# Kernel optimization log

Measured on AMD Instinct MI355X. Metric: run time of the kernel, lower is better.

Reference implementation:

```python
import jax, jax.numpy as jnp
import numpy as np

GRID = 64
AABB_MIN = np.array([-1.25, -1.55, -1.25], dtype=np.float32)
AABB_MAX = np.array([1.25, 0.95, 1.25], dtype=np.float32)
DENSITY_THRESH = 0.5


def setup_inputs() -> dict:
    key = jax.random.key(0)
    ks = jax.random.split(key, 12)
    N, S, H = 8192, 128, 64
    rays_o = jax.random.normal(ks[0], (N, 3), jnp.float32) * 0.1
    d = jax.random.normal(ks[1], (N, 3), jnp.float32)
    rays_d = d / jnp.sqrt(jnp.clip(jnp.sum(d * d, -1, keepdims=True), 1e-20))
    near = 0.05 + jax.random.uniform(ks[2], (N,), jnp.float32) * 0.5
    far = near + 2.0 + jax.random.uniform(ks[3], (N,), jnp.float32) * 0.5
    jitter = jax.random.uniform(ks[4], (N, S), jnp.float32)
    density_field = jax.random.uniform(ks[5], (GRID, GRID, GRID), jnp.float32)
    W1 = jax.random.normal(ks[6], (3, H), jnp.float32) * 0.5
    b1 = jnp.zeros((H,), jnp.float32)
    W2 = jax.random.normal(ks[7], (H, H), jnp.float32) * (1.0 / np.sqrt(H))
    b2 = jnp.zeros((H,), jnp.float32)
    Wsig = jax.random.normal(ks[8], (H, 1), jnp.float32) * (1.0 / np.sqrt(H))
    bsig = jnp.zeros((1,), jnp.float32)
    Wrgb = jax.random.normal(ks[9], (H, 3), jnp.float32) * (1.0 / np.sqrt(H))
    brgb = jnp.zeros((3,), jnp.float32)
    return {"rays_o": rays_o, "rays_d": rays_d, "near": near, "far": far,
            "jitter": jitter, "density_field": density_field,
            "W1": W1, "b1": b1, "W2": W2, "b2": b2,
            "Wsig": Wsig, "bsig": bsig, "Wrgb": Wrgb, "brgb": brgb}


def _render_train(rays_o, rays_d, near, far, jitter, density_field,
                  W1, b1, W2, b2, Wsig, bsig, Wrgb, brgb):
    N, S = jitter.shape
    step = (far - near) / S                                  # [N]
    offset = jnp.asarray(AABB_MIN)
    scale = jnp.asarray(AABB_MAX) - jnp.asarray(AABB_MIN)
    # uniform march (raymarch_train): z_i = near + i*step, zeroed where grid empty
    z = near[:, None] + jnp.arange(S, dtype=jnp.float32)[None, :] * step[:, None]  # [N,S]
    pts0 = rays_o[:, None, :] + z[..., None] * rays_d[:, None, :]                  # [N,S,3]
    u = (pts0 - offset) / scale
    idx = jnp.floor(u * GRID).astype(jnp.int32)
    inb = jnp.all((idx >= 0) & (idx < GRID), axis=-1)
    idxc = jnp.clip(idx, 0, GRID - 1)
    occ = density_field[idxc[..., 0], idxc[..., 1], idxc[..., 2]] > DENSITY_THRESH
    z_vals = jnp.where(occ & inb, z, 0.0)                    # [N,S]
    mask = z_vals > 0
    # stratified jitter (torch: z_vals + rand * step_size)
    z_vals = z_vals + jitter * step[:, None]
    pts = rays_o[:, None, :] + z_vals[..., None] * rays_d[:, None, :]  # [N,S,3]
    # radiance-field MLP (stand-in for `model(pts, None)`)
    h = jax.nn.relu(jnp.einsum('nsc,ch->nsh', pts, W1) + b1)
    h = jax.nn.relu(jnp.einsum('nsh,hk->nsk', h, W2) + b2)
    sigma = (jnp.einsum('nsh,ho->nso', h, Wsig) + bsig)[..., 0]        # [N,S]
    rgb = jax.nn.sigmoid(jnp.einsum('nsh,ho->nso', h, Wrgb) + brgb)    # [N,S,3]
    # torch fills masked-out samples with sigma=-1000, rgb=0
    sigma = jnp.where(mask, sigma, -1000.0)
    rgb = jnp.where(mask[..., None], rgb, 0.0)
    # composite
    dists = jnp.broadcast_to(step[:, None], sigma.shape)
    tau = jax.nn.relu(sigma) * dists
    alpha = 1.0 - jnp.exp(-tau)
    trans = jnp.concatenate([jnp.ones_like(alpha[..., :1]),
                             jnp.cumprod(1.0 - alpha + 1e-10, axis=-1)], axis=-1)
    w = alpha * trans[..., :-1]                              # [N,S]
    no_hit = trans[..., -1]
    color = jnp.sum(w[..., None] * rgb, axis=-2) + no_hit[..., None]   # bg_color=None -> white
    depth = jnp.sum(w * z_vals, axis=-1)
    return color, depth


def reference(rays_o, rays_d, near, far, jitter, density_field,
              W1, b1, W2, b2, Wsig, bsig, Wrgb, brgb):
    color, depth = _render_train(rays_o, rays_d, near, far, jitter, density_field,
                                 W1, b1, W2, b2, Wsig, bsig, Wrgb, brgb)
    return color
```

## Files before the change

kernel.cpp:

```cpp
#include <hip/hip_runtime.h>
#include <math.h>

#define S 128
#define H 64
#define RPB 4
#define SPB (RPB * S)
#define T 256

typedef __attribute__((ext_vector_type(8))) short bf16x8;
typedef __attribute__((ext_vector_type(4))) float f32x4;
#define MFMA16(a, b, c) __builtin_amdgcn_mfma_f32_16x16x32_bf16((a), (b), (c), 0, 0, 0)

__device__ __forceinline__ short f2bf(float x) {
    unsigned u = __float_as_uint(x);
    unsigned r = (u + 0x7fffu + ((u >> 16) & 1u)) >> 16;
    return (short)r;
}

__device__ __forceinline__ bool sample_mask(
    float ox, float oy, float oz, float dx, float dy, float dz,
    float nr, float step, int s, const float* __restrict__ density)
{
    const float z  = __fadd_rn(nr, __fmul_rn((float)s, step));
    const float px = __fadd_rn(ox, __fmul_rn(z, dx));
    const float py = __fadd_rn(oy, __fmul_rn(z, dy));
    const float pz = __fadd_rn(oz, __fmul_rn(z, dz));
    const float gx = floorf(__fmul_rn(__fdiv_rn(__fsub_rn(px, -1.25f), 2.5f), 64.0f));
    const float gy = floorf(__fmul_rn(__fdiv_rn(__fsub_rn(py, -1.55f), 2.5f), 64.0f));
    const float gz = floorf(__fmul_rn(__fdiv_rn(__fsub_rn(pz, -1.25f), 2.5f), 64.0f));
    const int ix = (int)gx, iy = (int)gy, iz = (int)gz;
    const bool inb = (ix >= 0) && (ix < 64) && (iy >= 0) && (iy < 64) &&
                     (iz >= 0) && (iz < 64);
    const int cx = min(max(ix, 0), 63);
    const int cy = min(max(iy, 0), 63);
    const int cz = min(max(iz, 0), 63);
    const float dval = density[(cx << 12) | (cy << 6) | cz];
    return inb && (dval > 0.5f);
}

__global__ __launch_bounds__(256)
void fused_mfma_kernel(const float* __restrict__ rays_o, const float* __restrict__ rays_d,
                       const float* __restrict__ nearv, const float* __restrict__ farv,
                       const float* __restrict__ jitter, const float* __restrict__ density,
                       const float* __restrict__ W1, const float* __restrict__ b1,
                       const float* __restrict__ W2, const float* __restrict__ b2,
                       const float* __restrict__ Wsig, const float* __restrict__ bsig,
                       const float* __restrict__ Wrgb, const float* __restrict__ brgb,
                       float* __restrict__ out, int N)
{
    __shared__ __align__(16) short sW2[H * 68];
    __shared__ __align__(16) short h1h[4][16 * 72];
    __shared__ __align__(16) short h2b[4][16 * 72];
    __shared__ unsigned short s_list[SPB];
    __shared__ float s_alpha[SPB];
    __shared__ float s_r[SPB], s_g[SPB], s_b[SPB];
    __shared__ int s_wcnt[4];
    __shared__ int s_wbase[4];

    const int tid  = threadIdx.x;
    const int lane = tid & 63;
    const int wv   = tid >> 6;
    const int blk  = blockIdx.x;
    const int mrow = lane & 15;
    const int quad = lane >> 4;

    for (int e = tid; e < H * H; e += T) {
        const int k = e >> 6, n = e & 63;
        sW2[k * 68 + n] = f2bf(W2[e]);
    }

    const int gr    = blk * RPB + wv;
    const int lbase = tid * 2;
    unsigned int mybits = 0u;
    if (gr < N) {
        const float ox = rays_o[gr * 3 + 0], oy = rays_o[gr * 3 + 1], oz = rays_o[gr * 3 + 2];
        const float dx = rays_d[gr * 3 + 0], dy = rays_d[gr * 3 + 1], dz = rays_d[gr * 3 + 2];
        const float nr = nearv[gr];
        const float step = __fdiv_rn(__fsub_rn(farv[gr], nr), 128.0f);
        const int s0 = lane * 2;
        #pragma unroll
        for (int j = 0; j < 2; ++j) {
            const bool m = sample_mask(ox, oy, oz, dx, dy, dz, nr, step, s0 + j, density);
            if (m) {
                mybits |= (1u << j);
            } else {
                s_alpha[lbase + j] = 0.0f;
                s_r[lbase + j] = 0.0f;
                s_g[lbase + j] = 0.0f;
                s_b[lbase + j] = 0.0f;
            }
        }
    } else {
        #pragma unroll
        for (int j = 0; j < 2; ++j) {
            s_alpha[lbase + j] = 0.0f;
            s_r[lbase + j] = 0.0f;
            s_g[lbase + j] = 0.0f;
            s_b[lbase + j] = 0.0f;
        }
    }
    const int mycnt = __popc(mybits);
    int inc = mycnt;
    #pragma unroll
    for (int off = 1; off < 64; off <<= 1) {
        const int u = __shfl_up(inc, off, 64);
        if (lane >= off) inc += u;
    }
    if (lane == 63) s_wcnt[wv] = inc;
    __syncthreads();
    if (tid == 0) {
        int t0 = 0;
        #pragma unroll
        for (int i = 0; i < 4; ++i) { s_wbase[i] = t0; t0 += s_wcnt[i]; }
    }
    __syncthreads();
    int pos = s_wbase[wv] + (inc - mycnt);
    if (mybits & 1u) s_list[pos++] = (unsigned short)lbase;
    if (mybits & 2u) s_list[pos]   = (unsigned short)(lbase + 1);
    __syncthreads();
    const int K = s_wbase[3] + s_wcnt[3];

    bf16x8 w2f[4][2];
    #pragma unroll
    for (int nt = 0; nt < 4; ++nt) {
        #pragma unroll
        for (int ks = 0; ks < 2; ++ks) {
            bf16x8 f;
            #pragma unroll
            for (int j = 0; j < 8; ++j)
                f[j] = sW2[(32 * ks + 8 * quad + j) * 68 + mrow + 16 * nt];
            w2f[nt][ks] = f;
        }
    }
    bf16x8 w1f[4];
    #pragma unroll
    for (int nt = 0; nt < 4; ++nt) {
        bf16x8 f = {0, 0, 0, 0, 0, 0, 0, 0};
        if (quad == 0) {
            const int n = mrow + 16 * nt;
            f[0] = f2bf(W1[n]);
            f[1] = f2bf(W1[64 + n]);
            f[2] = f2bf(W1[128 + n]);
        }
        w1f[nt] = f;
    }
    bf16x8 a3f[2];
    #pragma unroll
    for (int ks = 0; ks < 2; ++ks) {
        bf16x8 f = {0, 0, 0, 0, 0, 0, 0, 0};
        if (mrow < 4) {
            #pragma unroll
            for (int j = 0; j < 8; ++j) {
                const int k = 32 * ks + 8 * quad + j;
                const float v = (mrow == 0) ? Wsig[k] : Wrgb[k * 3 + (mrow - 1)];
                f[j] = f2bf(v);
            }
        }
        a3f[ks] = f;
    }
    float b1v[4], b2v[4];
    #pragma unroll
    for (int nt = 0; nt < 4; ++nt) {
        b1v[nt] = b1[mrow + 16 * nt];
        b2v[nt] = b2[mrow + 16 * nt];
    }
    const float bsg = bsig[0];
    const float br0 = brgb[0], br1 = brgb[1], br2 = brgb[2];

    const f32x4 z4 = {0.f, 0.f, 0.f, 0.f};
    const int ntask = (K + 15) >> 4;
    short* const hb = &h1h[wv][0];
    short* const gb = &h2b[wv][0];

    for (int t = wv; t < ntask; t += 4) {
        const int slot = (t << 4) + mrow;
        const bool valid = slot < K;
        const int id = s_list[valid ? slot : 0];
        const int r = blk * RPB + (id >> 7);
        const int s = id & (S - 1);
        const float nr = nearv[r];
        const float step = __fdiv_rn(__fsub_rn(farv[r], nr), 128.0f);
        const float zs = __fadd_rn(nr, __fmul_rn((float)s, step));
        const float zj = zs + jitter[blk * SPB + id] * step;
        const float qx = rays_o[r * 3 + 0] + zj * rays_d[r * 3 + 0];
        const float qy = rays_o[r * 3 + 1] + zj * rays_d[r * 3 + 1];
        const float qz = rays_o[r * 3 + 2] + zj * rays_d[r * 3 + 2];

        bf16x8 ah = {0, 0, 0, 0, 0, 0, 0, 0};
        if (quad == 0) { ah[0] = f2bf(qx); ah[1] = f2bf(qy); ah[2] = f2bf(qz); }
        #pragma unroll
        for (int nt = 0; nt < 4; ++nt) {
            const f32x4 c1 = MFMA16(ah, w1f[nt], z4);
            #pragma unroll
            for (int rg = 0; rg < 4; ++rg) {
                const float v = fmaxf(c1[rg] + b1v[nt], 0.0f);
                hb[(4 * quad + rg) * 72 + mrow + 16 * nt] = f2bf(v);
            }
        }

        bf16x8 a2_0 = *(const bf16x8*)&hb[mrow * 72 + 8 * quad];
        bf16x8 a2_1 = *(const bf16x8*)&hb[mrow * 72 + 32 + 8 * quad];
        #pragma unroll
        for (int nt = 0; nt < 4; ++nt) {
            const f32x4 c2 = MFMA16(a2_1, w2f[nt][1], MFMA16(a2_0, w2f[nt][0], z4));
            #pragma unroll
            for (int rg = 0; rg < 4; ++rg) {
                const float v = fmaxf(c2[rg] + b2v[nt], 0.0f);
                gb[(4 * quad + rg) * 72 + mrow + 16 * nt] = f2bf(v);
            }
        }

        bf16x8 b3_0 = *(const bf16x8*)&gb[mrow * 72 + 8 * quad];
        bf16x8 b3_1 = *(const bf16x8*)&gb[mrow * 72 + 32 + 8 * quad];
        const f32x4 c3 = MFMA16(a3f[1], b3_1, MFMA16(a3f[0], b3_0, z4));

        if (quad == 0 && valid) {
            const float sg = c3[0] + bsg;
            const float tau = fmaxf(sg, 0.0f) * step;
            s_alpha[id] = 1.0f - expf(-tau);
            s_r[id] = 1.0f / (1.0f + expf(-(c3[1] + br0)));
            s_g[id] = 1.0f / (1.0f + expf(-(c3[2] + br1)));
            s_b[id] = 1.0f / (1.0f + expf(-(c3[3] + br2)));
        }
    }
    __syncthreads();

    if (gr < N) {
        const int b0 = wv * S + 2 * lane;
        const float2 a01 = *reinterpret_cast<const float2*>(&s_alpha[b0]);
        const float a0 = a01.x, a1 = a01.y;
        const float t0 = (1.0f - a0) + 1e-10f;
        const float t1 = (1.0f - a1) + 1e-10f;
        float v = t0 * t1;
        #pragma unroll
        for (int off = 1; off < 64; off <<= 1) {
            const float u = __shfl_up(v, off, 64);
            if (lane >= off) v *= u;
        }
        float excl = __shfl_up(v, 1, 64);
        if (lane == 0) excl = 1.0f;
        const float no_hit = __shfl(v, 63, 64);
        const float w0 = a0 * excl;
        const float w1 = a1 * (excl * t0);
        const float2 r01 = *reinterpret_cast<const float2*>(&s_r[b0]);
        const float2 g01 = *reinterpret_cast<const float2*>(&s_g[b0]);
        const float2 b01 = *reinterpret_cast<const float2*>(&s_b[b0]);
        float cr = w0 * r01.x + w1 * r01.y;
        float cg = w0 * g01.x + w1 * g01.y;
        float cb = w0 * b01.x + w1 * b01.y;
        #pragma unroll
        for (int off = 32; off >= 1; off >>= 1) {
            cr += __shfl_xor(cr, off, 64);
            cg += __shfl_xor(cg, off, 64);
            cb += __shfl_xor(cb, off, 64);
        }
        if (lane == 0) {
            out[gr * 3 + 0] = cr + no_hit;
            out[gr * 3 + 1] = cg + no_hit;
            out[gr * 3 + 2] = cb + no_hit;
        }
    }
}

extern "C" void kernel_launch(void* const* d_in, const int* in_sizes, int n_in,
                              void* d_out, int out_size, void* d_ws, size_t ws_size,
                              hipStream_t stream) {
    const float* rays_o  = (const float*)d_in[0];
    const float* rays_d  = (const float*)d_in[1];
    const float* nearv   = (const float*)d_in[2];
    const float* farv    = (const float*)d_in[3];
    const float* jitter  = (const float*)d_in[4];
    const float* density = (const float*)d_in[5];
    const float* W1      = (const float*)d_in[6];
    const float* b1      = (const float*)d_in[7];
    const float* W2      = (const float*)d_in[8];
    const float* b2      = (const float*)d_in[9];
    const float* Wsig    = (const float*)d_in[10];
    const float* bsig    = (const float*)d_in[11];
    const float* Wrgb    = (const float*)d_in[12];
    const float* brgb    = (const float*)d_in[13];
    float* out = (float*)d_out;

    const int N = in_sizes[2];

    fused_mfma_kernel<<<dim3((N + RPB - 1) / RPB), dim3(T), 0, stream>>>(
        rays_o, rays_d, nearv, farv, jitter, density,
        W1, b1, W2, b2, Wsig, bsig, Wrgb, brgb, out, N);
}
```

Measured before the change: 109.5 us.

## Process eight rays per block and transpose W2 in LDS for vector loads

Doubles the rays handled per block so each thread builds masks for four samples, and each wave composites several rays. The per-block cost of converting W2 to bf16 and loading weight fragments is paid once for twice as much work. W2 is now stored transposed in shared memory, so each MFMA B-fragment comes from one 16-byte read instead of eight scalar reads. The two hidden-layer staging buffers are merged into one to save LDS. The trade-off is half as many blocks, fewer waves available to hide latency, and more shared memory per block for the larger sample arrays.

```diff
diff --git a/kernel.cpp b/kernel.cpp
--- a/kernel.cpp
+++ b/kernel.cpp
@@ -3,7 +3,7 @@
 
 #define S 128
 #define H 64
-#define RPB 4
+#define RPB 8
 #define SPB (RPB * S)
 #define T 256
 
@@ -48,9 +48,8 @@
                        const float* __restrict__ Wrgb, const float* __restrict__ brgb,
                        float* __restrict__ out, int N)
 {
-    __shared__ __align__(16) short sW2[H * 68];
-    __shared__ __align__(16) short h1h[4][16 * 72];
-    __shared__ __align__(16) short h2b[4][16 * 72];
+    __shared__ __align__(16) short sW2t[H * 72];
+    __shared__ __align__(16) short hX[4][16 * 72];
     __shared__ unsigned short s_list[SPB];
     __shared__ float s_alpha[SPB];
     __shared__ float s_r[SPB], s_g[SPB], s_b[SPB];
@@ -66,20 +65,20 @@
 
     for (int e = tid; e < H * H; e += T) {
         const int k = e >> 6, n = e & 63;
-        sW2[k * 68 + n] = f2bf(W2[e]);
-    }
-
-    const int gr    = blk * RPB + wv;
-    const int lbase = tid * 2;
+        sW2t[n * 72 + k] = f2bf(W2[e]);
+    }
+
+    const int lbase = tid * 4;
+    const int gra   = blk * RPB + (lbase >> 7);
     unsigned int mybits = 0u;
-    if (gr < N) {
-        const float ox = rays_o[gr * 3 + 0], oy = rays_o[gr * 3 + 1], oz = rays_o[gr * 3 + 2];
-        const float dx = rays_d[gr * 3 + 0], dy = rays_d[gr * 3 + 1], dz = rays_d[gr * 3 + 2];
-        const float nr = nearv[gr];
-        const float step = __fdiv_rn(__fsub_rn(farv[gr], nr), 128.0f);
-        const int s0 = lane * 2;
-        #pragma unroll
-        for (int j = 0; j < 2; ++j) {
+    if (gra < N) {
+        const float ox = rays_o[gra * 3 + 0], oy = rays_o[gra * 3 + 1], oz = rays_o[gra * 3 + 2];
+        const float dx = rays_d[gra * 3 + 0], dy = rays_d[gra * 3 + 1], dz = rays_d[gra * 3 + 2];
+        const float nr = nearv[gra];
+        const float step = __fdiv_rn(__fsub_rn(farv[gra], nr), 128.0f);
+        const int s0 = lbase & (S - 1);
+        #pragma unroll
+        for (int j = 0; j < 4; ++j) {
             const bool m = sample_mask(ox, oy, oz, dx, dy, dz, nr, step, s0 + j, density);
             if (m) {
                 mybits |= (1u << j);
@@ -92,7 +91,7 @@
         }
     } else {
         #pragma unroll
-        for (int j = 0; j < 2; ++j) {
+        for (int j = 0; j < 4; ++j) {
             s_alpha[lbase + j] = 0.0f;
             s_r[lbase + j] = 0.0f;
             s_g[lbase + j] = 0.0f;
@@ -115,8 +114,10 @@
     }
     __syncthreads();
     int pos = s_wbase[wv] + (inc - mycnt);
-    if (mybits & 1u) s_list[pos++] = (unsigned short)lbase;
-    if (mybits & 2u) s_list[pos]   = (unsigned short)(lbase + 1);
+    #pragma unroll
+    for (int j = 0; j < 4; ++j) {
+        if ((mybits >> j) & 1u) s_list[pos++] = (unsigned short)(lbase + j);
+    }
     __syncthreads();
     const int K = s_wbase[3] + s_wcnt[3];
 
@@ -125,11 +126,7 @@
     for (int nt = 0; nt < 4; ++nt) {
         #pragma unroll
         for (int ks = 0; ks < 2; ++ks) {
-            bf16x8 f;
-            #pragma unroll
-            for (int j = 0; j < 8; ++j)
-                f[j] = sW2[(32 * ks + 8 * quad + j) * 68 + mrow + 16 * nt];
-            w2f[nt][ks] = f;
+            w2f[nt][ks] = *(const bf16x8*)&sW2t[(mrow + 16 * nt) * 72 + 32 * ks + 8 * quad];
         }
     }
     bf16x8 w1f[4];
@@ -169,8 +166,7 @@
 
     const f32x4 z4 = {0.f, 0.f, 0.f, 0.f};
     const int ntask = (K + 15) >> 4;
-    short* const hb = &h1h[wv][0];
-    short* const gb = &h2b[wv][0];
+    short* const hb = &hX[wv][0];
 
     for (int t = wv; t < ntask; t += 4) {
         const int slot = (t << 4) + mrow;
@@ -206,12 +202,12 @@
             #pragma unroll
             for (int rg = 0; rg < 4; ++rg) {
                 const float v = fmaxf(c2[rg] + b2v[nt], 0.0f);
-                gb[(4 * quad + rg) * 72 + mrow + 16 * nt] = f2bf(v);
-            }
-        }
-
-        bf16x8 b3_0 = *(const bf16x8*)&gb[mrow * 72 + 8 * quad];
-        bf16x8 b3_1 = *(const bf16x8*)&gb[mrow * 72 + 32 + 8 * quad];
+                hb[(4 * quad + rg) * 72 + mrow + 16 * nt] = f2bf(v);
+            }
+        }
+
+        bf16x8 b3_0 = *(const bf16x8*)&hb[mrow * 72 + 8 * quad];
+        bf16x8 b3_1 = *(const bf16x8*)&hb[mrow * 72 + 32 + 8 * quad];
         const f32x4 c3 = MFMA16(a3f[1], b3_1, MFMA16(a3f[0], b3_0, z4));
 
         if (quad == 0 && valid) {
@@ -225,8 +221,11 @@
     }
     __syncthreads();
 
-    if (gr < N) {
-        const int b0 = wv * S + 2 * lane;
+    #pragma unroll
+    for (int ri = wv; ri < RPB; ri += 4) {
+        const int gr = blk * RPB + ri;
+        if (gr >= N) break;
+        const int b0 = ri * S + 2 * lane;
         const float2 a01 = *reinterpret_cast<const float2*>(&s_alpha[b0]);
         const float a0 = a01.x, a1 = a01.y;
         const float t0 = (1.0f - a0) + 1e-10f;
```

After: 105.2 us. 3.9% less time.
